# Optimization experiments

Hardware: AMD Instinct MI355X
Metric: run time of the kernel (lower is better)

The kernel has to match this reference:

```python
import jax, jax.numpy as jnp
import numpy as np
from itertools import product

N_VOX = 100000
GRID = 128
KS = 3
K = KS ** 3
INC_MAX, OUTC_MAX = 64, 96
RUNTIME_INC, RUNTIME_OUTC = 48, 64


def _build_rulebook(rng):
    flat = rng.choice(GRID ** 3, size=N_VOX, replace=False).astype(np.int64)
    coords = np.stack(np.unravel_index(flat, (GRID, GRID, GRID)), axis=1)  # [N,3]
    # Dense lookup table: flat coord -> voxel index (or -1).
    table = np.full(GRID ** 3, -1, dtype=np.int32)
    table[flat] = np.arange(N_VOX, dtype=np.int32)
    offsets = np.array(list(product([-1, 0, 1], repeat=3)), dtype=np.int64)  # [27,3]
    idx = np.empty((K, N_VOX), dtype=np.int32)
    for k, off in enumerate(offsets):
        nb = coords + off  # stride=1, dilation=1
        valid = np.all((nb >= 0) & (nb < GRID), axis=1)
        nb_flat = (nb[:, 0] * GRID + nb[:, 1]) * GRID + nb[:, 2]
        nb_flat = np.where(valid, nb_flat, 0)
        idx[k] = np.where(valid, table[nb_flat], -1)
    return idx


def setup_inputs() -> dict:
    key = jax.random.key(0)
    kf, kw = jax.random.split(key)
    features = jax.random.normal(kf, (N_VOX, RUNTIME_INC), dtype=jnp.float32)
    # Full kernel param [K, inc_max, outc_max]; runtime-sliced inside reference.
    std = 1.0 / np.sqrt(INC_MAX * K)
    kernel = jax.random.uniform(kw, (K, INC_MAX, OUTC_MAX), dtype=jnp.float32,
                                minval=-std, maxval=std)
    idx = jnp.asarray(_build_rulebook(np.random.default_rng(0)))  # [K, N]
    return {"features": features, "kernel": kernel, "idx": idx,
            "runtime_inc": RUNTIME_INC, "runtime_outc": RUNTIME_OUTC}


def reference(features, kernel, idx, runtime_inc, runtime_outc):
    # Dynamic channel slicing (static Python ints -> jit friendly).
    w = kernel[:, :runtime_inc, :runtime_outc]          # [K, Ci, Co]
    mask = idx >= 0                                      # [K, N]
    safe = jnp.where(mask, idx, 0)
    # Gather -> per-offset GEMM -> accumulate (scatter is identity: out idx == n).
    gathered = features[safe] * mask[..., None].astype(features.dtype)  # [K, N, Ci]
    out = jnp.einsum('knc,kco->no', gathered, w)         # [N, Co]
    return out
```

## Files before the change

### kernel.cpp

```cpp
#include <hip/hip_runtime.h>
#include <hip/hip_bf16.h>


#define NVOX       100000
#define INC        48
#define INC_MAX    64
#define OUTC       64
#define OUTC_MAX   96
#define KOFF       27
#define FEAT_ROW   64
#define FEATB_ELEMS (NVOX * FEAT_ROW)
#define WTB_ELEMS  (KOFF * 4096)
#define WS_NEED    ((size_t)(FEATB_ELEMS + WTB_ELEMS) * 2)
#define FEAT_PREP_BLKS 3125
#define WTB_PREP_BLKS  432
#define MAIN_BLOCKS 782

typedef __attribute__((ext_vector_type(8))) short  short8;
typedef __attribute__((ext_vector_type(4))) float  floatx4;

__device__ __forceinline__ short f2bf(float f) {
    union { __hip_bfloat16 h; short s; } u;
    u.h = __float2bfloat16(f);
    return u.s;
}

__global__ void __launch_bounds__(256)
prep_cvt(const float* __restrict__ feat, const float* __restrict__ wk,
         short* __restrict__ featb, short* __restrict__ wtb)
{
    int b = blockIdx.x;
    if (b < FEAT_PREP_BLKS) {
        int t = b * 256 + threadIdx.x;
        int g = t >> 3, c8 = (t & 7) * 8;
        short8 p = (short8){0, 0, 0, 0, 0, 0, 0, 0};
        if (c8 < INC) {
            const floatx4* src = (const floatx4*)(feat + g * INC + c8);
            floatx4 f0 = src[0], f1 = src[1];
            #pragma unroll
            for (int j = 0; j < 4; ++j) { p[j] = f2bf(f0[j]); p[4 + j] = f2bf(f1[j]); }
        }
        *(short8*)(featb + g * FEAT_ROW + c8) = p;
    } else {
        int t = (b - FEAT_PREP_BLKS) * 256 + threadIdx.x;
        int k = t >> 12, r = t & 4095;
        int frag = r >> 9, lane = (r >> 3) & 63, j = t & 7;
        int ks = frag >> 2, nt = frag & 3, quad = lane >> 4, l16 = lane & 15;
        int o = nt * 16 + l16, c = ks * 32 + quad * 8 + j;
        wtb[t] = (c < INC) ? f2bf(wk[k * (INC_MAX * OUTC_MAX) + c * OUTC_MAX + o])
                           : (short)0;
    }
}

__global__ void __launch_bounds__(256, 3)
spconv_main(const short* __restrict__ featb, const short* __restrict__ wtb,
            const int* __restrict__ idx, float* __restrict__ out)
{
    __shared__ short Bs[2][4096];

    const int tid  = threadIdx.x;
    const int lane = tid & 63;
    const int wave = tid >> 6;
    const int quad = lane >> 4;
    const int l16  = lane & 15;

    int bid = blockIdx.x;
    int sb  = (bid < 776) ? ((bid & 7) * 97 + (bid >> 3)) : bid;

    const int m0 = (sb * 4 + wave) * 32;
    const int r0 = m0 + l16;
    const int r1 = m0 + 16 + l16;
    const bool v0 = r0 < NVOX, v1 = r1 < NVOX;

    const short8 z8 = (short8){0, 0, 0, 0, 0, 0, 0, 0};

    floatx4 acc[2][4];
    #pragma unroll
    for (int i = 0; i < 2; ++i)
        #pragma unroll
        for (int j = 0; j < 4; ++j)
            acc[i][j] = (floatx4){0.f, 0.f, 0.f, 0.f};

    short8 a[2][2][2];

    auto aload = [&](short8 dst[2][2], int g0, int g1) {
        const short8* p0 = (const short8*)(featb + (g0 < 0 ? 0 : g0) * FEAT_ROW);
        const short8* p1 = (const short8*)(featb + (g1 < 0 ? 0 : g1) * FEAT_ROW);
        short8 t00 = p0[quad], t01 = p0[quad + 4];
        short8 t10 = p1[quad], t11 = p1[quad + 4];
        dst[0][0] = (g0 < 0) ? z8 : t00;  dst[0][1] = (g0 < 0) ? z8 : t01;
        dst[1][0] = (g1 < 0) ? z8 : t10;  dst[1][1] = (g1 < 0) ? z8 : t11;
    };

    int g0c = v0 ? idx[r0] : -1;
    int g1c = v1 ? idx[r1] : -1;
    int g0n = v0 ? idx[NVOX + r0] : -1;
    int g1n = v1 ? idx[NVOX + r1] : -1;
    aload(a[0], g0c, g1c);
    short8 bst0 = *(const short8*)(wtb + tid * 8);
    short8 bst1 = *(const short8*)(wtb + tid * 8 + 2048);

    #pragma unroll
    for (int k = 0; k < KOFF; ++k) {
        *(short8*)&Bs[k & 1][tid * 8]        = bst0;
        *(short8*)&Bs[k & 1][tid * 8 + 2048] = bst1;
        __syncthreads();

        if (k + 1 < KOFF) {
            bst0 = *(const short8*)(wtb + (k + 1) * 4096 + tid * 8);
            bst1 = *(const short8*)(wtb + (k + 1) * 4096 + tid * 8 + 2048);
            aload(a[(k + 1) & 1], g0n, g1n);
        }
        int g0f = -1, g1f = -1;
        if (k + 2 < KOFF) {
            g0f = v0 ? idx[(k + 2) * NVOX + r0] : -1;
            g1f = v1 ? idx[(k + 2) * NVOX + r1] : -1;
        }

        short8 b[2][4];
        #pragma unroll
        for (int ks = 0; ks < 2; ++ks)
            #pragma unroll
            for (int nt = 0; nt < 4; ++nt)
                b[ks][nt] = *(const short8*)&Bs[k & 1][(ks * 4 + nt) * 512 + lane * 8];

        #pragma unroll
        for (int ks = 0; ks < 2; ++ks)
            #pragma unroll
            for (int mt = 0; mt < 2; ++mt)
                #pragma unroll
                for (int nt = 0; nt < 4; ++nt)
                    acc[mt][nt] = __builtin_amdgcn_mfma_f32_16x16x32_bf16(
                        a[k & 1][mt][ks], b[ks][nt], acc[mt][nt], 0, 0, 0);

        g0n = g0f; g1n = g1f;
    }

    #pragma unroll
    for (int mt = 0; mt < 2; ++mt) {
        int gbase = m0 + mt * 16 + quad * 4;
        #pragma unroll
        for (int r = 0; r < 4; ++r) {
            if (gbase + r < NVOX) {
                #pragma unroll
                for (int nt = 0; nt < 4; ++nt)
                    out[(gbase + r) * OUTC + nt * 16 + l16] = acc[mt][nt][r];
            }
        }
    }
}

__global__ void __launch_bounds__(256)
spconv_fallback(const float* __restrict__ feat, const float* __restrict__ wk,
                const int* __restrict__ idx, float* __restrict__ out)
{
    int t = blockIdx.x * 256 + threadIdx.x;
    if (t >= NVOX * OUTC) return;
    int n = t >> 6, o = t & 63;
    float s = 0.f;
    for (int k = 0; k < KOFF; ++k) {
        int g = idx[k * NVOX + n];
        if (g >= 0) {
            const float* fr = feat + g * INC;
            const float* wr = wk + k * (INC_MAX * OUTC_MAX) + o;
            #pragma unroll 8
            for (int c = 0; c < INC; ++c) s += fr[c] * wr[c * OUTC_MAX];
        }
    }
    out[t] = s;
}

extern "C" void kernel_launch(void* const* d_in, const int* in_sizes, int n_in,
                              void* d_out, int out_size, void* d_ws, size_t ws_size,
                              hipStream_t stream) {
    const float* feat = (const float*)d_in[0];
    const float* wk   = (const float*)d_in[1];
    const int*   idx  = (const int*)d_in[2];
    float* out = (float*)d_out;

    if (ws_size >= WS_NEED) {
        short* featb = (short*)d_ws;
        short* wtb   = featb + FEATB_ELEMS;
        prep_cvt<<<FEAT_PREP_BLKS + WTB_PREP_BLKS, 256, 0, stream>>>(feat, wk, featb, wtb);
        spconv_main<<<MAIN_BLOCKS, 256, 0, stream>>>(featb, wtb, idx, out);
    } else {
        spconv_fallback<<<(NVOX * OUTC + 255) / 256, 256, 0, stream>>>(feat, wk, idx, out);
    }
}
```

Baseline: 115.4 us.

## Process two kernel offsets per barrier with deeper gather prefetch and zero-row padding

Restructures the main loop so each iteration stages weights for two kernel offsets into LDS, which halves the number of __syncthreads barriers. Gathered feature rows and weights are prefetched two offsets ahead, and indices four offsets ahead. Invalid neighbours are redirected to an extra all-zero row appended to the bf16 feature buffer, removing the per-load select. The cost is more registers for the deeper prefetch buffers and double the LDS per block, which may reduce occupancy at 3 blocks per SM.

```diff
diff --git a/kernel.cpp b/kernel.cpp
--- a/kernel.cpp
+++ b/kernel.cpp
@@ -9,10 +9,11 @@
 #define OUTC_MAX   96
 #define KOFF       27
 #define FEAT_ROW   64
-#define FEATB_ELEMS (NVOX * FEAT_ROW)
+#define FEATB_ELEMS ((NVOX + 1) * FEAT_ROW)
 #define WTB_ELEMS  (KOFF * 4096)
 #define WS_NEED    ((size_t)(FEATB_ELEMS + WTB_ELEMS) * 2)
-#define FEAT_PREP_BLKS 3125
+#define FEAT_THREADS ((NVOX + 1) * 8)
+#define FEAT_PREP_BLKS ((FEAT_THREADS + 255) / 256)
 #define WTB_PREP_BLKS  432
 #define MAIN_BLOCKS 782
 
@@ -32,15 +33,17 @@
     int b = blockIdx.x;
     if (b < FEAT_PREP_BLKS) {
         int t = b * 256 + threadIdx.x;
-        int g = t >> 3, c8 = (t & 7) * 8;
-        short8 p = (short8){0, 0, 0, 0, 0, 0, 0, 0};
-        if (c8 < INC) {
-            const floatx4* src = (const floatx4*)(feat + g * INC + c8);
-            floatx4 f0 = src[0], f1 = src[1];
-            #pragma unroll
-            for (int j = 0; j < 4; ++j) { p[j] = f2bf(f0[j]); p[4 + j] = f2bf(f1[j]); }
+        if (t < FEAT_THREADS) {
+            int g = t >> 3, c8 = (t & 7) * 8;
+            short8 p = (short8){0, 0, 0, 0, 0, 0, 0, 0};
+            if (g < NVOX && c8 < INC) {
+                const floatx4* src = (const floatx4*)(feat + g * INC + c8);
+                floatx4 f0 = src[0], f1 = src[1];
+                #pragma unroll
+                for (int j = 0; j < 4; ++j) { p[j] = f2bf(f0[j]); p[4 + j] = f2bf(f1[j]); }
+            }
+            *(short8*)(featb + g * FEAT_ROW + c8) = p;
         }
-        *(short8*)(featb + g * FEAT_ROW + c8) = p;
     } else {
         int t = (b - FEAT_PREP_BLKS) * 256 + threadIdx.x;
         int k = t >> 12, r = t & 4095;
@@ -56,7 +59,7 @@
 spconv_main(const short* __restrict__ featb, const short* __restrict__ wtb,
             const int* __restrict__ idx, float* __restrict__ out)
 {
-    __shared__ short Bs[2][4096];
+    __shared__ short Bs[2][2][4096];
 
     const int tid  = threadIdx.x;
     const int lane = tid & 63;
@@ -71,8 +74,8 @@
     const int r0 = m0 + l16;
     const int r1 = m0 + 16 + l16;
     const bool v0 = r0 < NVOX, v1 = r1 < NVOX;
-
-    const short8 z8 = (short8){0, 0, 0, 0, 0, 0, 0, 0};
+    const int rr0 = v0 ? r0 : 0;
+    const int rr1 = v1 ? r1 : 0;
 
     floatx4 acc[2][4];
     #pragma unroll
@@ -81,59 +84,66 @@
         for (int j = 0; j < 4; ++j)
             acc[i][j] = (floatx4){0.f, 0.f, 0.f, 0.f};
 
-    short8 a[2][2][2];
+    short8 A[4][2][2];
+    short8 bst[4][2];
+    int    row0[4], row1[4];
 
-    auto aload = [&](short8 dst[2][2], int g0, int g1) {
-        const short8* p0 = (const short8*)(featb + (g0 < 0 ? 0 : g0) * FEAT_ROW);
-        const short8* p1 = (const short8*)(featb + (g1 < 0 ? 0 : g1) * FEAT_ROW);
-        short8 t00 = p0[quad], t01 = p0[quad + 4];
-        short8 t10 = p1[quad], t11 = p1[quad + 4];
-        dst[0][0] = (g0 < 0) ? z8 : t00;  dst[0][1] = (g0 < 0) ? z8 : t01;
-        dst[1][0] = (g1 < 0) ? z8 : t10;  dst[1][1] = (g1 < 0) ? z8 : t11;
+    auto ldrow = [&](int k) {
+        int t0 = idx[k * NVOX + rr0];
+        int t1 = idx[k * NVOX + rr1];
+        row0[k & 3] = (t0 < 0) ? NVOX : t0;
+        row1[k & 3] = (t1 < 0) ? NVOX : t1;
     };
-
-    int g0c = v0 ? idx[r0] : -1;
-    int g1c = v1 ? idx[r1] : -1;
-    int g0n = v0 ? idx[NVOX + r0] : -1;
-    int g1n = v1 ? idx[NVOX + r1] : -1;
-    aload(a[0], g0c, g1c);
-    short8 bst0 = *(const short8*)(wtb + tid * 8);
-    short8 bst1 = *(const short8*)(wtb + tid * 8 + 2048);
-
-    #pragma unroll
-    for (int k = 0; k < KOFF; ++k) {
-        *(short8*)&Bs[k & 1][tid * 8]        = bst0;
-        *(short8*)&Bs[k & 1][tid * 8 + 2048] = bst1;
-        __syncthreads();
-
-        if (k + 1 < KOFF) {
-            bst0 = *(const short8*)(wtb + (k + 1) * 4096 + tid * 8);
-            bst1 = *(const short8*)(wtb + (k + 1) * 4096 + tid * 8 + 2048);
-            aload(a[(k + 1) & 1], g0n, g1n);
-        }
-        int g0f = -1, g1f = -1;
-        if (k + 2 < KOFF) {
-            g0f = v0 ? idx[(k + 2) * NVOX + r0] : -1;
-            g1f = v1 ? idx[(k + 2) * NVOX + r1] : -1;
-        }
-
-        short8 b[2][4];
+    auto aload = [&](int k) {
+        const short8* p0 = (const short8*)(featb + row0[k & 3] * FEAT_ROW);
+        const short8* p1 = (const short8*)(featb + row1[k & 3] * FEAT_ROW);
+        A[k & 3][0][0] = p0[quad];  A[k & 3][0][1] = p0[quad + 4];
+        A[k & 3][1][0] = p1[quad];  A[k & 3][1][1] = p1[quad + 4];
+    };
+    auto bload = [&](int k) {
+        bst[k & 3][0] = *(const short8*)(wtb + k * 4096 + tid * 8);
+        bst[k & 3][1] = *(const short8*)(wtb + k * 4096 + tid * 8 + 2048);
+    };
+    auto compute = [&](int k, int pb, int sub) {
         #pragma unroll
-        for (int ks = 0; ks < 2; ++ks)
+        for (int ks = 0; ks < 2; ++ks) {
+            short8 b[4];
             #pragma unroll
             for (int nt = 0; nt < 4; ++nt)
-                b[ks][nt] = *(const short8*)&Bs[k & 1][(ks * 4 + nt) * 512 + lane * 8];
-
-        #pragma unroll
-        for (int ks = 0; ks < 2; ++ks)
+                b[nt] = *(const short8*)&Bs[pb][sub][(ks * 4 + nt) * 512 + lane * 8];
             #pragma unroll
             for (int mt = 0; mt < 2; ++mt)
                 #pragma unroll
                 for (int nt = 0; nt < 4; ++nt)
                     acc[mt][nt] = __builtin_amdgcn_mfma_f32_16x16x32_bf16(
-                        a[k & 1][mt][ks], b[ks][nt], acc[mt][nt], 0, 0, 0);
+                        A[k & 3][mt][ks], b[nt], acc[mt][nt], 0, 0, 0);
+        }
+    };
 
-        g0n = g0f; g1n = g1f;
+    ldrow(0); ldrow(1); ldrow(2); ldrow(3);
+    aload(0); aload(1);
+    bload(0); bload(1);
+
+    #pragma unroll
+    for (int j = 0; j < 14; ++j) {
+        const int kk = 2 * j;
+        const int pb = j & 1;
+
+        *(short8*)&Bs[pb][0][tid * 8]        = bst[kk & 3][0];
+        *(short8*)&Bs[pb][0][tid * 8 + 2048] = bst[kk & 3][1];
+        if (kk + 1 < KOFF) {
+            *(short8*)&Bs[pb][1][tid * 8]        = bst[(kk + 1) & 3][0];
+            *(short8*)&Bs[pb][1][tid * 8 + 2048] = bst[(kk + 1) & 3][1];
+        }
+        __syncthreads();
+
+        if (kk + 2 < KOFF) { aload(kk + 2); bload(kk + 2); }
+        if (kk + 3 < KOFF) { aload(kk + 3); bload(kk + 3); }
+        if (kk + 4 < KOFF) ldrow(kk + 4);
+        if (kk + 5 < KOFF) ldrow(kk + 5);
+
+        compute(kk, pb, 0);
+        if (kk + 1 < KOFF) compute(kk + 1, pb, 1);
     }
 
     #pragma unroll
```

New measurement: 115.0 us. Within noise of the previous version (-0.3%).
